# Optimization experiments

Measured on AMD Instinct MI355X. Metric: run time of the kernel, lower is better.

## Reference

```python
import jax, jax.numpy as jnp
import numpy as np

NUM_HEADS = 4
IN_CHANNELS = 128


def setup_inputs() -> dict:
    key = jax.random.key(0)
    k_x, k_wq, k_bq, k_wo, k_bo = jax.random.split(key, 5)
    b, c, h, w = 16, IN_CHANNELS, 32, 32
    x = jax.random.normal(k_x, (b, c, h, w), dtype=jnp.float32)
    # 1x1 convs stored as (out_ch, in_ch) matrices
    w_qkv = jax.random.normal(k_wq, (c * 3 * NUM_HEADS, c), dtype=jnp.float32) * 0.02
    b_qkv = jax.random.normal(k_bq, (c * 3 * NUM_HEADS,), dtype=jnp.float32) * 0.02
    w_out = jax.random.normal(k_wo, (c, c * NUM_HEADS), dtype=jnp.float32) * 0.02
    b_out = jax.random.normal(k_bo, (c,), dtype=jnp.float32) * 0.02
    return {"x": x, "w_qkv": w_qkv, "b_qkv": b_qkv, "w_out": w_out, "b_out": b_out}


def reference(x, w_qkv, b_qkv, w_out, b_out):
    b, c, h, w = x.shape
    nh = NUM_HEADS
    # norm is Identity. 1x1 conv == per-pixel matmul over channels.
    qkv = jnp.einsum('bchw,oc->bohw', x, w_qkv) + b_qkv[None, :, None, None]
    qkv = qkv.reshape(b, nh, 3 * c, h, w)
    q, k, v = qkv[:, :, :c], qkv[:, :, c:2 * c], qkv[:, :, 2 * c:]
    # q, v: (b, nh, c, h, w) -> (b*nh, h*w, c); k -> (b*nh, c, h*w)
    q = q.transpose(0, 1, 3, 4, 2).reshape(b * nh, h * w, c)
    k = k.reshape(b * nh, c, h * w)
    v = v.transpose(0, 1, 3, 4, 2).reshape(b * nh, h * w, c)
    scores = jnp.einsum('bnc,bcm->bnm', q, k) * (c ** -0.5)  # (b*nh, hw, hw)
    attn = jax.nn.softmax(scores, axis=-1)
    out = jnp.einsum('bnm,bmc->bnc', attn, v)  # (b*nh, hw, c)
    out = out.reshape(b, nh, h, w, c).transpose(0, 4, 1, 2, 3).reshape(b, nh * c, h, w)
    out = jnp.einsum('bchw,oc->bohw', out, w_out) + b_out[None, :, None, None]
    return out + x
```

## Files before the change

### kernel.cpp

```cpp
#include <hip/hip_runtime.h>
#include <hip/hip_bf16.h>

typedef float  f32x4_v   __attribute__((ext_vector_type(4)));
typedef float  f32x16_v  __attribute__((ext_vector_type(16)));
typedef __bf16 bf16x8_v  __attribute__((ext_vector_type(8)));
typedef __bf16 bf16x4_v  __attribute__((ext_vector_type(4)));

#define WS_Q  0
#define WS_K  8388608
#define WS_V  16777216
#define WS_O  25165824
#define WS_WP 33554432

__device__ __forceinline__ int aswz(int p) { return ((p & 7) ^ ((p >> 3) & 7)) << 4; }

__device__ __forceinline__ void gload16(const void* g, void* l) {
    __builtin_amdgcn_global_load_lds(
        (const __attribute__((address_space(1))) unsigned int*)g,
        (__attribute__((address_space(3))) unsigned int*)l, 16, 0, 0);
}

__global__ __launch_bounds__(256) void k_qkv(const float* __restrict__ x,
                                             const float* __restrict__ w_qkv,
                                             const float* __restrict__ b_qkv,
                                             __bf16* __restrict__ q_ws,
                                             __bf16* __restrict__ k_ws,
                                             __bf16* __restrict__ v_ws,
                                             const float* __restrict__ w_out,
                                             __bf16* __restrict__ w_frag) {
    __shared__ __bf16 Ash[128 * 128];
    __shared__ __bf16 Bsh[128 * 128];
    const int tid  = threadIdx.x;
    const int quar = blockIdx.x;
    const int mt   = blockIdx.y;
    const int gm0  = mt * 128;
    const int b    = gm0 >> 10;
    const int p0   = gm0 & 1023;

    if (quar < 2) {
        int gid  = (mt * 2 + quar) * 256 + tid;
        int e    = gid & 7;
        int colo = (gid >> 3) & 31;
        int hi   = (gid >> 8) & 1;
        int ks   = (gid >> 9) & 7;
        int ot   = (gid >> 12) & 3;
        int head = gid >> 14;
        int o    = ot * 32 + colo;
        int c    = ks * 16 + hi * 8 + e;
        w_frag[gid] = (__bf16)w_out[o * 512 + c * 4 + head];
    }

    char* Ab = reinterpret_cast<char*>(Ash);
    char* Bb = reinterpret_cast<char*>(Bsh);

    for (int it = 0; it < 16; ++it) {
        int idx = tid + it * 256;
        int c   = idx >> 5;
        int i4  = (idx & 31) << 2;
        float4 v = *reinterpret_cast<const float4*>(x + b * 131072 + c * 1024 + p0 + i4);
        float vv[4] = {v.x, v.y, v.z, v.w};
#pragma unroll
        for (int j = 0; j < 4; ++j) {
            int p = i4 + j;
            int byte = ((p << 8) | (c << 1)) ^ aswz(p);
            *reinterpret_cast<__bf16*>(Ab + byte) = (__bf16)vv[j];
        }
    }

    const int lane = tid & 63;
    const int wv   = tid >> 6;
    const int wm   = (wv >> 1) * 64;
    const int wn   = (wv & 1) * 64;
    const int lr   = lane & 15;
    const int lg   = lane >> 4;
    const int bh   = b * 4 + quar;

    for (int i = 0; i < 3; ++i) {
        const int o0 = (quar * 3 + i) * 128;
        __syncthreads();
        for (int it = 0; it < 16; ++it) {
            int idx = tid + it * 256;
            int o   = idx >> 5;
            int c4  = (idx & 31) << 2;
            float4 v = *reinterpret_cast<const float4*>(w_qkv + (o0 + o) * 128 + c4);
            bf16x4_v h;
            h[0] = (__bf16)v.x; h[1] = (__bf16)v.y; h[2] = (__bf16)v.z; h[3] = (__bf16)v.w;
            int byte = ((o << 8) | (c4 << 1)) ^ aswz(o);
            *reinterpret_cast<bf16x4_v*>(Bb + byte) = h;
        }
        __syncthreads();

        if (i == 2) {
            f32x4_v acc[4][4] = {};
#pragma unroll
            for (int ks = 0; ks < 4; ++ks) {
                bf16x8_v af[4], bfr[4];
#pragma unroll
                for (int mi = 0; mi < 4; ++mi) {
                    int row  = wm + mi * 16 + lr;
                    int byte = ((row << 8) | (ks << 6) | (lg << 4)) ^ aswz(row);
                    af[mi] = *reinterpret_cast<const bf16x8_v*>(Ab + byte);
                }
#pragma unroll
                for (int ni = 0; ni < 4; ++ni) {
                    int row  = wn + ni * 16 + lr;
                    int byte = ((row << 8) | (ks << 6) | (lg << 4)) ^ aswz(row);
                    bfr[ni] = *reinterpret_cast<const bf16x8_v*>(Bb + byte);
                }
#pragma unroll
                for (int mi = 0; mi < 4; ++mi)
#pragma unroll
                    for (int ni = 0; ni < 4; ++ni)
                        acc[mi][ni] = __builtin_amdgcn_mfma_f32_16x16x32_bf16(af[mi], bfr[ni], acc[mi][ni], 0, 0, 0);
            }
#pragma unroll
            for (int ni = 0; ni < 4; ++ni) {
                int ch   = wn + ni * 16 + lr;
                float bias = b_qkv[o0 + ch];
#pragma unroll
                for (int mi = 0; mi < 4; ++mi) {
                    int prow = p0 + wm + mi * 16 + lg * 4;
                    bf16x4_v hv;
#pragma unroll
                    for (int r = 0; r < 4; ++r) hv[r] = (__bf16)(acc[mi][ni][r] + bias);
                    int addr = bh * 131072 + (prow >> 5) * 4096 +
                               ((ch >> 5) * 2 + ((prow >> 4) & 1)) * 512 +
                               ((prow >> 3) & 1) * 256 + (ch & 31) * 8 + (prow & 7);
                    *reinterpret_cast<bf16x4_v*>(&v_ws[addr]) = hv;
                }
            }
        } else {
            f32x4_v acc[4][4] = {};
#pragma unroll
            for (int ks = 0; ks < 4; ++ks) {
                bf16x8_v af[4], bfr[4];
#pragma unroll
                for (int mi = 0; mi < 4; ++mi) {
                    int row  = wm + mi * 16 + lr;
                    int byte = ((row << 8) | (ks << 6) | (lg << 4)) ^ aswz(row);
                    af[mi] = *reinterpret_cast<const bf16x8_v*>(Ab + byte);
                }
#pragma unroll
                for (int ni = 0; ni < 4; ++ni) {
                    int row  = wn + ni * 16 + lr;
                    int byte = ((row << 8) | (ks << 6) | (lg << 4)) ^ aswz(row);
                    bfr[ni] = *reinterpret_cast<const bf16x8_v*>(Bb + byte);
                }
#pragma unroll
                for (int ni = 0; ni < 4; ++ni)
#pragma unroll
                    for (int mi = 0; mi < 4; ++mi)
                        acc[ni][mi] = __builtin_amdgcn_mfma_f32_16x16x32_bf16(bfr[ni], af[mi], acc[ni][mi], 0, 0, 0);
            }
            __bf16* dst = (i == 0 ? q_ws : k_ws) + bh * 131072;
            const float sc = (i == 0) ? 0.12751744f : 1.0f;
#pragma unroll
            for (int ni = 0; ni < 4; ++ni) {
                int chb = wn + ni * 16 + lg * 4;
                float4 b4 = *reinterpret_cast<const float4*>(&b_qkv[o0 + chb]);
                float bias[4] = {b4.x, b4.y, b4.z, b4.w};
#pragma unroll
                for (int mi = 0; mi < 4; ++mi) {
                    int p = p0 + wm + mi * 16 + lr;
                    bf16x4_v hv;
#pragma unroll
                    for (int r = 0; r < 4; ++r)
                        hv[r] = (__bf16)((acc[ni][mi][r] + bias[r]) * sc);
                    int off = (p >> 5) * 4096 + (chb >> 4) * 512 +
                              ((chb >> 3) & 1) * 256 + (p & 31) * 8 + (chb & 7);
                    *reinterpret_cast<bf16x4_v*>(dst + off) = hv;
                }
            }
        }
    }
}

__global__ __launch_bounds__(512, 2) void k_attn(const __bf16* __restrict__ q_ws,
                                                 const __bf16* __restrict__ k_ws,
                                                 const __bf16* __restrict__ v_ws,
                                                 __bf16* __restrict__ o_ws) {
    __shared__ __bf16 Kbuf[2][8192];
    __shared__ __bf16 Vbuf[2][8192];

    const int tid  = threadIdx.x;
    const int lane = tid & 63;
    const int wv   = tid >> 6;
    const int col  = lane & 31;
    const int hi   = lane >> 5;

    const int id   = blockIdx.x;
    const int bh   = (id & 7) * 8 + (id >> 5);
    const int qt   = (id >> 3) & 3;
    const int base = bh * 131072;
    const int q0w  = qt * 256 + wv * 32;

    const char* kfb = reinterpret_cast<const char*>(k_ws + base);
    const char* vfb = reinterpret_cast<const char*>(v_ws + base);
    const int lane16 = lane * 16;
    const char* sfb = (wv < 4) ? kfb : vfb;
    const int   cw  = (wv & 3) * 4;

    {
        char* db = (wv < 4) ? (char*)&Kbuf[0][0] : (char*)&Vbuf[0][0];
#pragma unroll
        for (int i = 0; i < 4; ++i)
            gload16(sfb + (cw + i) * 1024 + lane16, db + (cw + i) * 1024);
    }
    bf16x8_v bq[8];
    {
        const __bf16* qp = q_ws + base + (q0w >> 5) * 4096 + lane * 8;
#pragma unroll
        for (int ks = 0; ks < 8; ++ks)
            bq[ks] = *reinterpret_cast<const bf16x8_v*>(qp + ks * 512);
    }
    asm volatile("s_waitcnt vmcnt(0)" ::: "memory");

    f32x16_v of[4] = {};
    float l = 0.f;

    for (int t = 0; t < 16; ++t) {
        const int cur = t & 1;
        const char* Kl = (const char*)&Kbuf[cur][0];
        const char* Vl = (const char*)&Vbuf[cur][0];

        __builtin_amdgcn_s_barrier();
        asm volatile("" ::: "memory");
        __builtin_amdgcn_sched_barrier(0);

        if (t < 15) {
            const char* sn = sfb + (t + 1) * 16384;
            char* dn = (wv < 4) ? (char*)&Kbuf[cur ^ 1][0] : (char*)&Vbuf[cur ^ 1][0];
#pragma unroll
            for (int i = 0; i < 4; ++i)
                gload16(sn + (cw + i) * 1024 + lane16, dn + (cw + i) * 1024);
            asm volatile("s_waitcnt vmcnt(4)" ::: "memory");
        } else {
            asm volatile("s_waitcnt vmcnt(0)" ::: "memory");
        }
        __builtin_amdgcn_sched_barrier(0);

        f32x16_v sa = {}, sb = {};
        __builtin_amdgcn_s_setprio(1);
#pragma unroll
        for (int ks = 0; ks < 8; ++ks) {
            bf16x8_v af0 = *reinterpret_cast<const bf16x8_v*>(Kl + ks * 1024 + lane16);
            bf16x8_v af1 = *reinterpret_cast<const bf16x8_v*>(Kl + (8 + ks) * 1024 + lane16);
            sa = __builtin_amdgcn_mfma_f32_32x32x16_bf16(af0, bq[ks], sa, 0, 0, 0);
            sb = __builtin_amdgcn_mfma_f32_32x32x16_bf16(af1, bq[ks], sb, 0, 0, 0);
        }
        __builtin_amdgcn_s_setprio(0);

        float rs = 0.f;
#pragma unroll
        for (int r = 0; r < 16; ++r) { sa[r] = __builtin_amdgcn_exp2f(sa[r]); rs += sa[r]; }
#pragma unroll
        for (int r = 0; r < 16; ++r) { sb[r] = __builtin_amdgcn_exp2f(sb[r]); rs += sb[r]; }
        l += rs + __shfl_xor(rs, 32);

        bf16x8_v pa[4];
#pragma unroll
        for (int j = 0; j < 4; ++j) {
            const f32x16_v& sj = (j < 2) ? sa : sb;
            const int ro = 8 * (j & 1);
            unsigned w0, w1, w2, w3;
            asm("v_cvt_pk_bf16_f32 %0, %1, %2" : "=v"(w0) : "v"(sj[ro + 0]), "v"(sj[ro + 1]));
            asm("v_cvt_pk_bf16_f32 %0, %1, %2" : "=v"(w2) : "v"(sj[ro + 4]), "v"(sj[ro + 5]));
            asm("v_cvt_pk_bf16_f32 %0, %1, %2" : "=v"(w1) : "v"(sj[ro + 2]), "v"(sj[ro + 3]));
            asm("v_cvt_pk_bf16_f32 %0, %1, %2" : "=v"(w3) : "v"(sj[ro + 6]), "v"(sj[ro + 7]));
            asm("v_permlane32_swap_b32 %0, %1" : "+v"(w0), "+v"(w2));
            asm("v_permlane32_swap_b32 %0, %1" : "+v"(w1), "+v"(w3));
            union { unsigned u[4]; bf16x8_v h; } cvt;
            cvt.u[0] = w0; cvt.u[1] = w1; cvt.u[2] = w2; cvt.u[3] = w3;
            pa[j] = cvt.h;
        }

        __builtin_amdgcn_s_setprio(1);
#pragma unroll
        for (int n = 0; n < 4; ++n) {
#pragma unroll
            for (int j = 0; j < 4; ++j) {
                bf16x8_v bv = *reinterpret_cast<const bf16x8_v*>(
                    Vl + (j >> 1) * 8192 + (n * 2 + (j & 1)) * 1024 + lane16);
                of[n] = __builtin_amdgcn_mfma_f32_32x32x16_bf16(pa[j], bv, of[n], 0, 0, 0);
            }
        }
        __builtin_amdgcn_s_setprio(0);

        asm volatile("s_waitcnt lgkmcnt(0)" ::: "memory");
        __builtin_amdgcn_sched_barrier(0);
    }

    float linv = 1.0f / l;
    const int obase = base + (q0w >> 5) * 4096;
#pragma unroll
    for (int r = 0; r < 16; ++r) {
        int qr = (r & 3) + 4 * hi + 8 * (r >> 2);
        float ld = __shfl(linv, qr);
#pragma unroll
        for (int n = 0; n < 4; ++n) {
            int addr = obase + (2 * n + (col >> 4)) * 512 + ((col >> 3) & 1) * 256 + qr * 8 + (col & 7);
            o_ws[addr] = (__bf16)(of[n][r] * ld);
        }
    }
}

__global__ __launch_bounds__(256, 2) void k_out(const __bf16* __restrict__ o_frag,
                                                const __bf16* __restrict__ w_frag,
                                                const float* __restrict__ b_out,
                                                const float* __restrict__ x,
                                                float* __restrict__ out) {
    const int tid  = threadIdx.x;
    const int lane = tid & 63;
    const int ot   = tid >> 6;
    const int col  = lane & 31;
    const int hi   = lane >> 5;
    const int bid  = blockIdx.x;
    const int b    = bid >> 5;
    const int pc   = bid & 31;

    const __bf16* wbase = w_frag + ot * 4096 + lane * 8;
    const __bf16* obase = o_frag + (b * 4) * 131072 + pc * 4096 + lane * 8;

    bf16x8_v awA[8], boA[8], awB[8], boB[8];
#pragma unroll
    for (int ks = 0; ks < 8; ++ks) {
        awA[ks] = *reinterpret_cast<const bf16x8_v*>(wbase + ks * 512);
        boA[ks] = *reinterpret_cast<const bf16x8_v*>(obase + ks * 512);
    }

    f32x16_v acc0 = {}, acc1 = {};
#pragma unroll
    for (int head = 0; head < 4; ++head) {
        bf16x8_v (&awC)[8] = (head & 1) ? awB : awA;
        bf16x8_v (&boC)[8] = (head & 1) ? boB : boA;
        bf16x8_v (&awN)[8] = (head & 1) ? awA : awB;
        bf16x8_v (&boN)[8] = (head & 1) ? boA : boB;
        if (head < 3) {
            const __bf16* wn = wbase + (head + 1) * 16384;
            const __bf16* on = obase + (head + 1) * 131072;
#pragma unroll
            for (int ks = 0; ks < 8; ++ks) {
                awN[ks] = *reinterpret_cast<const bf16x8_v*>(wn + ks * 512);
                boN[ks] = *reinterpret_cast<const bf16x8_v*>(on + ks * 512);
            }
        }
        f32x16_v& acc = (head < 2) ? acc0 : acc1;
#pragma unroll
        for (int ks = 0; ks < 8; ++ks)
            acc = __builtin_amdgcn_mfma_f32_32x32x16_bf16(awC[ks], boC[ks], acc, 0, 0, 0);
    }

#pragma unroll
    for (int r = 0; r < 16; ++r) {
        int o = ot * 32 + (r & 3) + 4 * hi + 8 * (r >> 2);
        int p = pc * 32 + col;
        int idx = b * 131072 + o * 1024 + p;
        out[idx] = acc0[r] + acc1[r] + b_out[o] + x[idx];
    }
}

extern "C" void kernel_launch(void* const* d_in, const int* in_sizes, int n_in,
                              void* d_out, int out_size, void* d_ws, size_t ws_size,
                              hipStream_t stream) {
    const float* x     = (const float*)d_in[0];
    const float* w_qkv = (const float*)d_in[1];
    const float* b_qkv = (const float*)d_in[2];
    const float* w_out = (const float*)d_in[3];
    const float* b_out = (const float*)d_in[4];
    float* out = (float*)d_out;
    __bf16* ws = (__bf16*)d_ws;

    __bf16* q_ws   = ws + WS_Q;
    __bf16* k_ws   = ws + WS_K;
    __bf16* v_ws   = ws + WS_V;
    __bf16* o_ws   = ws + WS_O;
    __bf16* w_frag = ws + WS_WP;

    k_qkv<<<dim3(4, 128), 256, 0, stream>>>(x, w_qkv, b_qkv, q_ws, k_ws, v_ws, w_out, w_frag);
    k_attn<<<256, 512, 0, stream>>>(q_ws, k_ws, v_ws, o_ws);
    k_out<<<512, 256, 0, stream>>>(o_ws, w_frag, b_out, x, out);
}
```

Measured before the change: 78.23 us.

## Software-pipeline the PV matmul one tile behind QK and exp in attention

The attention loop now runs the P·V MFMAs for the previous key tile right after the current tile's QK MFMAs, before the exp and bf16 conversion. This lets the exp and pack work overlap with matrix-core work instead of following it in series. The V tile now needs three LDS buffers so the previous tile stays live while the next one is loaded, and a drain step after the loop handles the last tile. The launch bound drops to one block per CU, which frees registers for the carried P fragments but may reduce occupancy.

```diff
diff --git a/kernel.cpp b/kernel.cpp
--- a/kernel.cpp
+++ b/kernel.cpp
@@ -175,12 +175,12 @@
     }
 }
 
-__global__ __launch_bounds__(512, 2) void k_attn(const __bf16* __restrict__ q_ws,
+__global__ __launch_bounds__(512, 1) void k_attn(const __bf16* __restrict__ q_ws,
                                                  const __bf16* __restrict__ k_ws,
                                                  const __bf16* __restrict__ v_ws,
                                                  __bf16* __restrict__ o_ws) {
     __shared__ __bf16 Kbuf[2][8192];
-    __shared__ __bf16 Vbuf[2][8192];
+    __shared__ __bf16 Vbuf[3][8192];
 
     const int tid  = threadIdx.x;
     const int lane = tid & 63;
@@ -217,11 +217,11 @@
 
     f32x16_v of[4] = {};
     float l = 0.f;
+    bf16x8_v paP[4];
 
     for (int t = 0; t < 16; ++t) {
-        const int cur = t & 1;
-        const char* Kl = (const char*)&Kbuf[cur][0];
-        const char* Vl = (const char*)&Vbuf[cur][0];
+        const char* Kl = (const char*)&Kbuf[t & 1][0];
+        const char* Vp = (const char*)&Vbuf[(t + 2) % 3][0];
 
         __builtin_amdgcn_s_barrier();
         asm volatile("" ::: "memory");
@@ -229,7 +229,8 @@
 
         if (t < 15) {
             const char* sn = sfb + (t + 1) * 16384;
-            char* dn = (wv < 4) ? (char*)&Kbuf[cur ^ 1][0] : (char*)&Vbuf[cur ^ 1][0];
+            char* dn = (wv < 4) ? (char*)&Kbuf[(t + 1) & 1][0]
+                                : (char*)&Vbuf[(t + 1) % 3][0];
 #pragma unroll
             for (int i = 0; i < 4; ++i)
                 gload16(sn + (cw + i) * 1024 + lane16, dn + (cw + i) * 1024);
@@ -250,6 +251,18 @@
         }
         __builtin_amdgcn_s_setprio(0);
 
+        if (t > 0) {
+#pragma unroll
+            for (int n = 0; n < 4; ++n) {
+#pragma unroll
+                for (int j = 0; j < 4; ++j) {
+                    bf16x8_v bv = *reinterpret_cast<const bf16x8_v*>(
+                        Vp + (j >> 1) * 8192 + (n * 2 + (j & 1)) * 1024 + lane16);
+                    of[n] = __builtin_amdgcn_mfma_f32_32x32x16_bf16(paP[j], bv, of[n], 0, 0, 0);
+                }
+            }
+        }
+
         float rs = 0.f;
 #pragma unroll
         for (int r = 0; r < 16; ++r) { sa[r] = __builtin_amdgcn_exp2f(sa[r]); rs += sa[r]; }
@@ -257,7 +270,6 @@
         for (int r = 0; r < 16; ++r) { sb[r] = __builtin_amdgcn_exp2f(sb[r]); rs += sb[r]; }
         l += rs + __shfl_xor(rs, 32);
 
-        bf16x8_v pa[4];
 #pragma unroll
         for (int j = 0; j < 4; ++j) {
             const f32x16_v& sj = (j < 2) ? sa : sb;
@@ -271,25 +283,25 @@
             asm("v_permlane32_swap_b32 %0, %1" : "+v"(w1), "+v"(w3));
             union { unsigned u[4]; bf16x8_v h; } cvt;
             cvt.u[0] = w0; cvt.u[1] = w1; cvt.u[2] = w2; cvt.u[3] = w3;
-            pa[j] = cvt.h;
-        }
-
-        __builtin_amdgcn_s_setprio(1);
+            paP[j] = cvt.h;
+        }
+
+        asm volatile("s_waitcnt lgkmcnt(0)" ::: "memory");
+        __builtin_amdgcn_sched_barrier(0);
+    }
+
+    {
+        const char* Vp = (const char*)&Vbuf[0][0];
 #pragma unroll
         for (int n = 0; n < 4; ++n) {
 #pragma unroll
             for (int j = 0; j < 4; ++j) {
                 bf16x8_v bv = *reinterpret_cast<const bf16x8_v*>(
-                    Vl + (j >> 1) * 8192 + (n * 2 + (j & 1)) * 1024 + lane16);
-                of[n] = __builtin_amdgcn_mfma_f32_32x32x16_bf16(pa[j], bv, of[n], 0, 0, 0);
-            }
-        }
-        __builtin_amdgcn_s_setprio(0);
-
-        asm volatile("s_waitcnt lgkmcnt(0)" ::: "memory");
-        __builtin_amdgcn_sched_barrier(0);
-    }
-
+                    Vp + (j >> 1) * 8192 + (n * 2 + (j & 1)) * 1024 + lane16);
+                of[n] = __builtin_amdgcn_mfma_f32_32x32x16_bf16(paP[j], bv, of[n], 0, 0, 0);
+            }
+        }
+    }
     float linv = 1.0f / l;
     const int obase = base + (q0w >> 5) * 4096;
 #pragma unroll
```

Result: no change. 76.84 us (median of 2 runs) (-1.8%).

## Fuse output projection into attention kernel with per-block all-heads tiles

Applied to the files above, without the earlier changes.

Merges the attention and output-projection kernels. Each block now covers all four heads of one batch for a 64-query tile, staging the normalized attention output in shared memory and applying the output 1x1 conv, bias and residual in place. This removes the bf16 O round-trip through global memory and one kernel launch. In exchange, each block uses 128KB of LDS, occupancy drops to one block per CU, and the KV loop runs 32 shorter steps with half the MFMA work per barrier, which may expose more latency.

```diff
diff --git a/kernel.cpp b/kernel.cpp
--- a/kernel.cpp
+++ b/kernel.cpp
@@ -9,7 +9,6 @@
 #define WS_Q  0
 #define WS_K  8388608
 #define WS_V  16777216
-#define WS_O  25165824
 #define WS_WP 33554432
 
 __device__ __forceinline__ int aswz(int p) { return ((p & 7) ^ ((p >> 3) & 7)) << 4; }
@@ -175,40 +174,42 @@
     }
 }
 
-__global__ __launch_bounds__(512, 2) void k_attn(const __bf16* __restrict__ q_ws,
+__global__ __launch_bounds__(512, 1) void k_attn(const __bf16* __restrict__ q_ws,
                                                  const __bf16* __restrict__ k_ws,
                                                  const __bf16* __restrict__ v_ws,
-                                                 __bf16* __restrict__ o_ws) {
-    __shared__ __bf16 Kbuf[2][8192];
-    __shared__ __bf16 Vbuf[2][8192];
+                                                 const __bf16* __restrict__ w_frag,
+                                                 const float* __restrict__ b_out,
+                                                 const float* __restrict__ x,
+                                                 float* __restrict__ out) {
+    __shared__ __bf16 SMEM[65536];
 
     const int tid  = threadIdx.x;
     const int lane = tid & 63;
     const int wv   = tid >> 6;
     const int col  = lane & 31;
     const int hi   = lane >> 5;
-
-    const int id   = blockIdx.x;
-    const int bh   = (id & 7) * 8 + (id >> 5);
-    const int qt   = (id >> 3) & 3;
-    const int base = bh * 131072;
-    const int q0w  = qt * 256 + wv * 32;
-
-    const char* kfb = reinterpret_cast<const char*>(k_ws + base);
-    const char* vfb = reinterpret_cast<const char*>(v_ws + base);
+    const int h    = wv & 3;
+    const int half = wv >> 2;
+
+    const int id = blockIdx.x;
+    const int b  = (id & 7) * 2 + (id >> 7);
+    const int qt = (id >> 3) & 15;
+    const int bh = b * 4 + h;
+
+    const char* kfb = reinterpret_cast<const char*>(k_ws) + (b * 4 + (wv & 3)) * 262144;
+    const char* vfb = reinterpret_cast<const char*>(v_ws) + (b * 4 + (wv & 3)) * 262144;
     const int lane16 = lane * 16;
     const char* sfb = (wv < 4) ? kfb : vfb;
-    const int   cw  = (wv & 3) * 4;
-
-    {
-        char* db = (wv < 4) ? (char*)&Kbuf[0][0] : (char*)&Vbuf[0][0];
-#pragma unroll
-        for (int i = 0; i < 4; ++i)
-            gload16(sfb + (cw + i) * 1024 + lane16, db + (cw + i) * 1024);
+    const int   dof = (wv < 4) ? (wv * 8192) : (32768 + (wv - 4) * 8192);
+
+#pragma unroll
+    for (int i = 0; i < 4; ++i) {
+        gload16(sfb + i * 2048 + lane16,        (char*)SMEM + dof + i * 2048);
+        gload16(sfb + i * 2048 + 1024 + lane16, (char*)SMEM + dof + i * 2048 + 1024);
     }
     bf16x8_v bq[8];
     {
-        const __bf16* qp = q_ws + base + (q0w >> 5) * 4096 + lane * 8;
+        const __bf16* qp = q_ws + bh * 131072 + (qt * 2 + half) * 4096 + lane * 8;
 #pragma unroll
         for (int ks = 0; ks < 8; ++ks)
             bq[ks] = *reinterpret_cast<const bf16x8_v*>(qp + ks * 512);
@@ -218,69 +219,65 @@
     f32x16_v of[4] = {};
     float l = 0.f;
 
-    for (int t = 0; t < 16; ++t) {
+    for (int t = 0; t < 32; ++t) {
         const int cur = t & 1;
-        const char* Kl = (const char*)&Kbuf[cur][0];
-        const char* Vl = (const char*)&Vbuf[cur][0];
+        const char* Kl = (const char*)SMEM + cur * 65536 + h * 8192;
+        const char* Vl = (const char*)SMEM + cur * 65536 + 32768 + h * 8192;
 
         __builtin_amdgcn_s_barrier();
         asm volatile("" ::: "memory");
         __builtin_amdgcn_sched_barrier(0);
 
-        if (t < 15) {
-            const char* sn = sfb + (t + 1) * 16384;
-            char* dn = (wv < 4) ? (char*)&Kbuf[cur ^ 1][0] : (char*)&Vbuf[cur ^ 1][0];
-#pragma unroll
-            for (int i = 0; i < 4; ++i)
-                gload16(sn + (cw + i) * 1024 + lane16, dn + (cw + i) * 1024);
-            asm volatile("s_waitcnt vmcnt(4)" ::: "memory");
+        if (t < 31) {
+            const char* sn = sfb + (t + 1) * 8192;
+            char* dn = (char*)SMEM + (cur ^ 1) * 65536 + dof;
+#pragma unroll
+            for (int i = 0; i < 4; ++i) {
+                gload16(sn + i * 2048 + lane16,        dn + i * 2048);
+                gload16(sn + i * 2048 + 1024 + lane16, dn + i * 2048 + 1024);
+            }
+            asm volatile("s_waitcnt vmcnt(8)" ::: "memory");
         } else {
             asm volatile("s_waitcnt vmcnt(0)" ::: "memory");
         }
         __builtin_amdgcn_sched_barrier(0);
 
-        f32x16_v sa = {}, sb = {};
+        f32x16_v sa = {};
         __builtin_amdgcn_s_setprio(1);
 #pragma unroll
         for (int ks = 0; ks < 8; ++ks) {
-            bf16x8_v af0 = *reinterpret_cast<const bf16x8_v*>(Kl + ks * 1024 + lane16);
-            bf16x8_v af1 = *reinterpret_cast<const bf16x8_v*>(Kl + (8 + ks) * 1024 + lane16);
-            sa = __builtin_amdgcn_mfma_f32_32x32x16_bf16(af0, bq[ks], sa, 0, 0, 0);
-            sb = __builtin_amdgcn_mfma_f32_32x32x16_bf16(af1, bq[ks], sb, 0, 0, 0);
+            bf16x8_v af = *reinterpret_cast<const bf16x8_v*>(Kl + ks * 1024 + lane16);
+            sa = __builtin_amdgcn_mfma_f32_32x32x16_bf16(af, bq[ks], sa, 0, 0, 0);
         }
         __builtin_amdgcn_s_setprio(0);
 
         float rs = 0.f;
 #pragma unroll
         for (int r = 0; r < 16; ++r) { sa[r] = __builtin_amdgcn_exp2f(sa[r]); rs += sa[r]; }
-#pragma unroll
-        for (int r = 0; r < 16; ++r) { sb[r] = __builtin_amdgcn_exp2f(sb[r]); rs += sb[r]; }
         l += rs + __shfl_xor(rs, 32);
 
-        bf16x8_v pa[4];
-#pragma unroll
-        for (int j = 0; j < 4; ++j) {
-            const f32x16_v& sj = (j < 2) ? sa : sb;
-            const int ro = 8 * (j & 1);
+        bf16x8_v pa[2];
+#pragma unroll
+        for (int j = 0; j < 2; ++j) {
+            const int ro = 8 * j;
             unsigned w0, w1, w2, w3;
-            asm("v_cvt_pk_bf16_f32 %0, %1, %2" : "=v"(w0) : "v"(sj[ro + 0]), "v"(sj[ro + 1]));
-            asm("v_cvt_pk_bf16_f32 %0, %1, %2" : "=v"(w2) : "v"(sj[ro + 4]), "v"(sj[ro + 5]));
-            asm("v_cvt_pk_bf16_f32 %0, %1, %2" : "=v"(w1) : "v"(sj[ro + 2]), "v"(sj[ro + 3]));
-            asm("v_cvt_pk_bf16_f32 %0, %1, %2" : "=v"(w3) : "v"(sj[ro + 6]), "v"(sj[ro + 7]));
+            asm("v_cvt_pk_bf16_f32 %0, %1, %2" : "=v"(w0) : "v"(sa[ro + 0]), "v"(sa[ro + 1]));
+            asm("v_cvt_pk_bf16_f32 %0, %1, %2" : "=v"(w2) : "v"(sa[ro + 4]), "v"(sa[ro + 5]));
+            asm("v_cvt_pk_bf16_f32 %0, %1, %2" : "=v"(w1) : "v"(sa[ro + 2]), "v"(sa[ro + 3]));
+            asm("v_cvt_pk_bf16_f32 %0, %1, %2" : "=v"(w3) : "v"(sa[ro + 6]), "v"(sa[ro + 7]));
             asm("v_permlane32_swap_b32 %0, %1" : "+v"(w0), "+v"(w2));
             asm("v_permlane32_swap_b32 %0, %1" : "+v"(w1), "+v"(w3));
-            union { unsigned u[4]; bf16x8_v h; } cvt;
+            union { unsigned u[4]; bf16x8_v h2; } cvt;
             cvt.u[0] = w0; cvt.u[1] = w1; cvt.u[2] = w2; cvt.u[3] = w3;
-            pa[j] = cvt.h;
+            pa[j] = cvt.h2;
         }
 
         __builtin_amdgcn_s_setprio(1);
 #pragma unroll
         for (int n = 0; n < 4; ++n) {
 #pragma unroll
-            for (int j = 0; j < 4; ++j) {
-                bf16x8_v bv = *reinterpret_cast<const bf16x8_v*>(
-                    Vl + (j >> 1) * 8192 + (n * 2 + (j & 1)) * 1024 + lane16);
+            for (int j = 0; j < 2; ++j) {
+                bf16x8_v bv = *reinterpret_cast<const bf16x8_v*>(Vl + (n * 2 + j) * 1024 + lane16);
                 of[n] = __builtin_amdgcn_mfma_f32_32x32x16_bf16(pa[j], bv, of[n], 0, 0, 0);
             }
         }
@@ -290,70 +287,42 @@
         __builtin_amdgcn_sched_barrier(0);
     }
 
-    float linv = 1.0f / l;
-    const int obase = base + (q0w >> 5) * 4096;
-#pragma unroll
-    for (int r = 0; r < 16; ++r) {
-        int qr = (r & 3) + 4 * hi + 8 * (r >> 2);
-        float ld = __shfl(linv, qr);
-#pragma unroll
-        for (int n = 0; n < 4; ++n) {
-            int addr = obase + (2 * n + (col >> 4)) * 512 + ((col >> 3) & 1) * 256 + qr * 8 + (col & 7);
-            o_ws[addr] = (__bf16)(of[n][r] * ld);
-        }
-    }
-}
-
-__global__ __launch_bounds__(256, 2) void k_out(const __bf16* __restrict__ o_frag,
-                                                const __bf16* __restrict__ w_frag,
-                                                const float* __restrict__ b_out,
-                                                const float* __restrict__ x,
-                                                float* __restrict__ out) {
-    const int tid  = threadIdx.x;
-    const int lane = tid & 63;
-    const int ot   = tid >> 6;
-    const int col  = lane & 31;
-    const int hi   = lane >> 5;
-    const int bid  = blockIdx.x;
-    const int b    = bid >> 5;
-    const int pc   = bid & 31;
-
-    const __bf16* wbase = w_frag + ot * 4096 + lane * 8;
-    const __bf16* obase = o_frag + (b * 4) * 131072 + pc * 4096 + lane * 8;
-
-    bf16x8_v awA[8], boA[8], awB[8], boB[8];
-#pragma unroll
-    for (int ks = 0; ks < 8; ++ks) {
-        awA[ks] = *reinterpret_cast<const bf16x8_v*>(wbase + ks * 512);
-        boA[ks] = *reinterpret_cast<const bf16x8_v*>(obase + ks * 512);
-    }
-
+    __builtin_amdgcn_s_barrier();
+    asm volatile("" ::: "memory");
+
+    {
+        float linv = 1.0f / l;
+#pragma unroll
+        for (int r = 0; r < 16; ++r) {
+            int qr = (r & 3) + 4 * hi + 8 * (r >> 2);
+            float ld = __shfl(linv, qr);
+            __bf16* orow = SMEM + half * 16640 + qr * 520 + h * 128 + col;
+#pragma unroll
+            for (int n = 0; n < 4; ++n)
+                orow[n * 32] = (__bf16)(of[n][r] * ld);
+        }
+    }
+    __syncthreads();
+
+    const int ot = wv & 3, qh = wv >> 2;
     f32x16_v acc0 = {}, acc1 = {};
-#pragma unroll
-    for (int head = 0; head < 4; ++head) {
-        bf16x8_v (&awC)[8] = (head & 1) ? awB : awA;
-        bf16x8_v (&boC)[8] = (head & 1) ? boB : boA;
-        bf16x8_v (&awN)[8] = (head & 1) ? awA : awB;
-        bf16x8_v (&boN)[8] = (head & 1) ? boA : boB;
-        if (head < 3) {
-            const __bf16* wn = wbase + (head + 1) * 16384;
-            const __bf16* on = obase + (head + 1) * 131072;
-#pragma unroll
-            for (int ks = 0; ks < 8; ++ks) {
-                awN[ks] = *reinterpret_cast<const bf16x8_v*>(wn + ks * 512);
-                boN[ks] = *reinterpret_cast<const bf16x8_v*>(on + ks * 512);
-            }
-        }
-        f32x16_v& acc = (head < 2) ? acc0 : acc1;
-#pragma unroll
-        for (int ks = 0; ks < 8; ++ks)
-            acc = __builtin_amdgcn_mfma_f32_32x32x16_bf16(awC[ks], boC[ks], acc, 0, 0, 0);
+    const __bf16* wb = w_frag + ot * 4096 + lane * 8;
+    const char* ob = (const char*)SMEM + qh * 33280 + col * 1040 + hi * 16;
+#pragma unroll
+    for (int hk = 0; hk < 4; ++hk) {
+        f32x16_v& acc = (hk < 2) ? acc0 : acc1;
+#pragma unroll
+        for (int ks = 0; ks < 8; ++ks) {
+            bf16x8_v aw = *reinterpret_cast<const bf16x8_v*>(wb + hk * 16384 + ks * 512);
+            bf16x8_v bo = *reinterpret_cast<const bf16x8_v*>(ob + hk * 256 + ks * 32);
+            acc = __builtin_amdgcn_mfma_f32_32x32x16_bf16(aw, bo, acc, 0, 0, 0);
+        }
     }
 
 #pragma unroll
     for (int r = 0; r < 16; ++r) {
         int o = ot * 32 + (r & 3) + 4 * hi + 8 * (r >> 2);
-        int p = pc * 32 + col;
+        int p = qt * 64 + qh * 32 + col;
         int idx = b * 131072 + o * 1024 + p;
         out[idx] = acc0[r] + acc1[r] + b_out[o] + x[idx];
     }
@@ -373,10 +342,8 @@
     __bf16* q_ws   = ws + WS_Q;
     __bf16* k_ws   = ws + WS_K;
     __bf16* v_ws   = ws + WS_V;
-    __bf16* o_ws   = ws + WS_O;
     __bf16* w_frag = ws + WS_WP;
 
     k_qkv<<<dim3(4, 128), 256, 0, stream>>>(x, w_qkv, b_qkv, q_ws, k_ws, v_ws, w_out, w_frag);
-    k_attn<<<256, 512, 0, stream>>>(q_ws, k_ws, v_ws, o_ws);
-    k_out<<<512, 256, 0, stream>>>(o_ws, w_frag, b_out, x, out);
+    k_attn<<<256, 512, 0, stream>>>(q_ws, k_ws, v_ws, w_frag, b_out, x, out);
 }
```

Result: slower. 81.23 us (+3.8%).
